# Kernel optimization log

Hardware: AMD Instinct MI355X
Metric: run time of the kernel (lower is better)

## Reference

```python
import jax, jax.numpy as jnp
import numpy as np

B, H, S, DK = 2, 16, 2048, 64


def setup_inputs() -> dict:
    key = jax.random.key(0)
    kq, kk, kv = jax.random.split(key, 3)
    Q = jax.random.normal(kq, (B, H, S, DK), dtype=jnp.float32)
    K = jax.random.normal(kk, (B, H, S, DK), dtype=jnp.float32)
    V = jax.random.normal(kv, (B, H, S, DK), dtype=jnp.float32)
    mask = jnp.tril(jnp.ones((S, S), dtype=bool))  # causal, broadcasts over (B, H)
    return {"Q": Q, "K": K, "V": V, "mask": mask}


def reference(Q, K, V, mask):
    d_k = Q.shape[-1]
    scale = 1.0 / jnp.sqrt(jnp.asarray(d_k, dtype=Q.dtype))
    # [..., m, n] attention scores
    qk = jnp.einsum("bhmd,bhnd->bhmn", Q, K) * scale
    qk = jnp.where(mask, qk, -jnp.inf)
    attn = jax.nn.softmax(qk, axis=-1)
    return jnp.einsum("bhmn,bhnd->bhmd", attn, V)
```

## Files before the change

kernel.cpp:

```cpp
#include <hip/hip_runtime.h>
#include <hip/hip_bf16.h>
#include <stdint.h>


#define SEQ   2048
#define DKK   64
#define KVB   64
#define NKT   (SEQ / KVB)
#define TILE_BYTES 16384
#define WS_NEED ((size_t)32 * NKT * TILE_BYTES)

typedef float  f32x4  __attribute__((ext_vector_type(4)));
typedef short  s16x8  __attribute__((ext_vector_type(8)));
typedef short  s16x4  __attribute__((ext_vector_type(4)));
typedef __bf16 bf16x8 __attribute__((ext_vector_type(8)));

static __device__ __forceinline__ unsigned short f2b(float x) {
  union { float f; uint32_t u; } v; v.f = x;
  uint32_t r = v.u + 0x7fffu + ((v.u >> 16) & 1u);
  return (unsigned short)(r >> 16);
}

static __device__ __forceinline__ int swzA(int row, int col) {
  return row * 128 + ((((col >> 3) ^ (row & 7)) << 4)) + ((col & 7) << 1);
}
static __device__ __forceinline__ int swzV(int d, int kv) {
  return d * 128 + ((((kv >> 3) ^ ((d >> 1) & 7)) << 4)) + ((kv & 7) << 1);
}

__global__ __launch_bounds__(256)
void prep_kv(const float* __restrict__ Kg, const float* __restrict__ Vg,
             char* __restrict__ ws) {
  const int b   = blockIdx.x;
  const int bh  = b >> 5, kt = b & 31;
  const int tid = threadIdx.x;
  char* tile = ws + ((size_t)b << 14);
  const size_t base = ((size_t)bh * SEQ + (size_t)kt * KVB) * DKK;
  const float* Kb = Kg + base;
  const float* Vb = Vg + base;
  {
    int col4 = tid & 15, rq = tid >> 4;
#pragma unroll
    for (int ii = 0; ii < 4; ++ii) {
      int row = ii * 16 + rq;
      f32x4 v = *(const f32x4*)(Kb + (size_t)row * DKK + col4 * 4);
      s16x4 w; w[0]=f2b(v[0]); w[1]=f2b(v[1]); w[2]=f2b(v[2]); w[3]=f2b(v[3]);
      *(s16x4*)(tile + swzA(row, col4 * 4)) = w;
    }
  }
  {
    int d0 = (tid & 15) * 4, kv0 = (tid >> 4) * 4;
    f32x4 vv[4];
#pragma unroll
    for (int r2 = 0; r2 < 4; ++r2)
      vv[r2] = *(const f32x4*)(Vb + (size_t)(kv0 + r2) * DKK + d0);
#pragma unroll
    for (int j = 0; j < 4; ++j) {
      s16x4 w; w[0]=f2b(vv[0][j]); w[1]=f2b(vv[1][j]); w[2]=f2b(vv[2][j]); w[3]=f2b(vv[3][j]);
      *(s16x4*)(tile + 8192 + swzV(d0 + j, kv0)) = w;
    }
  }
}

__global__ __launch_bounds__(256, 2)
void attn_fwd5(const float* __restrict__ Qg, const char* __restrict__ ws,
               float* __restrict__ Og) {
  __shared__ __align__(16) char smem[TILE_BYTES + 4 * 2048];

  const int tid  = threadIdx.x;
  const int lane = tid & 63;
  const int wave = tid >> 6;
  const int c    = lane & 15;
  const int g    = lane >> 4;

  const int f     = blockIdx.x;
  const int xcd   = f & 7;
  const int inner = f >> 3;
  const int bh    = ((inner >> 4) << 3) | xcd;
  const int p     = inner & 15;
  const int qt_a  = 31 - p;
  const int qt_b  = p;
  const int nkt_a = qt_a + 1;
  const int nkt_b = qt_b + 1;

  const float CS = 0.18033688011f;
  const size_t bhoff = (size_t)bh * SEQ * DKK;
  const float* Qb = Qg + bhoff;
  float*       Ob = Og + bhoff;
  const char*  wsb = ws + ((size_t)bh * NKT << 14);

  s16x8 stA0 = *(const s16x8*)(wsb + tid * 16);
  s16x8 stA1 = *(const s16x8*)(wsb + 4096 + tid * 16);
  s16x8 stB0 = *(const s16x8*)(wsb + 8192 + tid * 16);
  s16x8 stB1 = *(const s16x8*)(wsb + 12288 + tid * 16);

  s16x8 qfA[2], qfB[2];
#pragma unroll
  for (int h = 0; h < 2; ++h) {
    int d0 = h * 32 + g * 8;
    {
      const f32x4* pq = (const f32x4*)(Qb + (size_t)(qt_a * 64 + wave * 16 + c) * DKK + d0);
      f32x4 a = pq[0], b = pq[1];
      s16x8 r;
      r[0]=f2b(a[0]*CS); r[1]=f2b(a[1]*CS); r[2]=f2b(a[2]*CS); r[3]=f2b(a[3]*CS);
      r[4]=f2b(b[0]*CS); r[5]=f2b(b[1]*CS); r[6]=f2b(b[2]*CS); r[7]=f2b(b[3]*CS);
      qfA[h] = r;
    }
    {
      const f32x4* pq = (const f32x4*)(Qb + (size_t)(qt_b * 64 + wave * 16 + c) * DKK + d0);
      f32x4 a = pq[0], b = pq[1];
      s16x8 r;
      r[0]=f2b(a[0]*CS); r[1]=f2b(a[1]*CS); r[2]=f2b(a[2]*CS); r[3]=f2b(a[3]*CS);
      r[4]=f2b(b[0]*CS); r[5]=f2b(b[1]*CS); r[6]=f2b(b[2]*CS); r[7]=f2b(b[3]*CS);
      qfB[h] = r;
    }
  }

  s16x8 ones8;
#pragma unroll
  for (int j = 0; j < 8; ++j) ones8[j] = (short)0x3F80;

  f32x4 OA[4] = {}, OB[4] = {};
  f32x4 OlA = {}, OlB = {};

  char* Kl = smem;
  char* Vl = smem + 8192;
  char* Pl = smem + TILE_BYTES + wave * 2048;

  auto compute_tile = [&](const s16x8* qf, f32x4* O, f32x4& Ol, bool domask) {
    f32x4 S[4] = {};
    __builtin_amdgcn_s_setprio(1);
#pragma unroll
    for (int s = 0; s < 4; ++s)
#pragma unroll
      for (int h = 0; h < 2; ++h) {
        s16x8 kf = *(const s16x8*)(Kl + swzA(s * 16 + c, h * 32 + g * 8));
        S[s] = __builtin_amdgcn_mfma_f32_16x16x32_bf16(
            __builtin_bit_cast(bf16x8, qf[h]),
            __builtin_bit_cast(bf16x8, kf), S[s], 0, 0, 0);
      }
    __builtin_amdgcn_s_setprio(0);

    if (domask) {
      int qrl = wave * 16 + g * 4;
#pragma unroll
      for (int s = 0; s < 4; ++s) {
        int kvl = s * 16 + c;
#pragma unroll
        for (int r = 0; r < 4; ++r)
          if (kvl > qrl + r) S[s][r] = -1e30f;
      }
    }

#pragma unroll
    for (int r = 0; r < 4; ++r)
#pragma unroll
      for (int s = 0; s < 4; ++s) {
        float pv = exp2f(S[s][r]);
        *(unsigned short*)(Pl + swzA(g * 4 + r, s * 16 + c)) = f2b(pv);
      }

    __builtin_amdgcn_s_setprio(1);
#pragma unroll
    for (int ch = 0; ch < 2; ++ch) {
      s16x8 pa = *(const s16x8*)(Pl + swzA(c, ch * 32 + g * 8));
#pragma unroll
      for (int t = 0; t < 4; ++t) {
        s16x8 vb = *(const s16x8*)(Vl + swzV(t * 16 + c, ch * 32 + g * 8));
        O[t] = __builtin_amdgcn_mfma_f32_16x16x32_bf16(
            __builtin_bit_cast(bf16x8, pa),
            __builtin_bit_cast(bf16x8, vb), O[t], 0, 0, 0);
      }
      Ol = __builtin_amdgcn_mfma_f32_16x16x32_bf16(
          __builtin_bit_cast(bf16x8, pa),
          __builtin_bit_cast(bf16x8, ones8), Ol, 0, 0, 0);
    }
    __builtin_amdgcn_s_setprio(0);
  };

  for (int kt = 0; kt < nkt_a; ++kt) {
    __syncthreads();
    *(s16x8*)(smem + tid * 16)         = stA0;
    *(s16x8*)(smem + 4096 + tid * 16)  = stA1;
    *(s16x8*)(smem + 8192 + tid * 16)  = stB0;
    *(s16x8*)(smem + 12288 + tid * 16) = stB1;
    if (kt + 1 < nkt_a) {
      const char* tn = wsb + ((size_t)(kt + 1) << 14);
      stA0 = *(const s16x8*)(tn + tid * 16);
      stA1 = *(const s16x8*)(tn + 4096 + tid * 16);
      stB0 = *(const s16x8*)(tn + 8192 + tid * 16);
      stB1 = *(const s16x8*)(tn + 12288 + tid * 16);
    }
    __syncthreads();

    compute_tile(qfA, OA, OlA, kt == qt_a);
    if (kt < nkt_b)
      compute_tile(qfB, OB, OlB, kt == qt_b);
  }

#pragma unroll
  for (int r = 0; r < 4; ++r) {
    int qra = qt_a * 64 + wave * 16 + g * 4 + r;
    int qrb = qt_b * 64 + wave * 16 + g * 4 + r;
    float ia = 1.f / OlA[r];
    float ib = 1.f / OlB[r];
#pragma unroll
    for (int t = 0; t < 4; ++t) {
      Ob[(size_t)qra * DKK + t * 16 + c] = OA[t][r] * ia;
      Ob[(size_t)qrb * DKK + t * 16 + c] = OB[t][r] * ib;
    }
  }
}

__global__ __launch_bounds__(256, 2)
void attn_fwd(const float* __restrict__ Qg, const float* __restrict__ Kg,
              const float* __restrict__ Vg, float* __restrict__ Og) {
  __shared__ __align__(16) char smem[8192 + 8192 + 8 * 2048];
  char* Kl = smem;
  char* Vl = smem + 8192;
  const int tid  = threadIdx.x;
  const int lane = tid & 63;
  const int wave = tid >> 6;
  const int c    = lane & 15;
  const int g    = lane >> 4;
  const int f    = blockIdx.x;
  const int xcd  = f & 7;
  const int inner= f >> 3;
  const int bh   = ((inner >> 4) << 3) | xcd;
  const int qt   = 15 - (inner & 15);
  const float CS = 0.18033688011f;
  const size_t bhoff = (size_t)bh * SEQ * DKK;
  const float* Qb = Qg + bhoff;
  const float* Kb = Kg + bhoff;
  const float* Vb = Vg + bhoff;
  float*       Ob = Og + bhoff;
  s16x8 qf[2][2];
#pragma unroll
  for (int u = 0; u < 2; ++u) {
    int qrow = qt * 128 + wave * 32 + u * 16 + c;
#pragma unroll
    for (int h = 0; h < 2; ++h) {
      int d0 = h * 32 + g * 8;
      const f32x4* pq = (const f32x4*)(Qb + (size_t)qrow * DKK + d0);
      f32x4 a = pq[0], b = pq[1];
      s16x8 r;
      r[0]=f2b(a[0]*CS); r[1]=f2b(a[1]*CS); r[2]=f2b(a[2]*CS); r[3]=f2b(a[3]*CS);
      r[4]=f2b(b[0]*CS); r[5]=f2b(b[1]*CS); r[6]=f2b(b[2]*CS); r[7]=f2b(b[3]*CS);
      qf[u][h] = r;
    }
  }
  f32x4 O[2][4] = {};
  float m[2][4], l[2][4];
#pragma unroll
  for (int u = 0; u < 2; ++u)
#pragma unroll
    for (int r = 0; r < 4; ++r) { m[u][r] = -1e30f; l[u][r] = 0.f; }
  const int nkt = 2 * qt + 2;
  for (int kt = 0; kt < nkt; ++kt) {
    __syncthreads();
    {
      int col4 = tid & 15, rq = tid >> 4;
#pragma unroll
      for (int ii = 0; ii < 4; ++ii) {
        int row = ii * 16 + rq;
        f32x4 v = *(const f32x4*)(Kb + (size_t)(kt * KVB + row) * DKK + col4 * 4);
        s16x4 w; w[0]=f2b(v[0]); w[1]=f2b(v[1]); w[2]=f2b(v[2]); w[3]=f2b(v[3]);
        *(s16x4*)(Kl + swzA(row, col4 * 4)) = w;
      }
      int d0 = (tid & 15) * 4, kv0 = (tid >> 4) * 4;
      f32x4 vv[4];
#pragma unroll
      for (int r2 = 0; r2 < 4; ++r2)
        vv[r2] = *(const f32x4*)(Vb + (size_t)(kt * KVB + kv0 + r2) * DKK + d0);
#pragma unroll
      for (int j = 0; j < 4; ++j) {
        s16x4 w; w[0]=f2b(vv[0][j]); w[1]=f2b(vv[1][j]); w[2]=f2b(vv[2][j]); w[3]=f2b(vv[3][j]);
        *(s16x4*)(Vl + swzV(d0 + j, kv0)) = w;
      }
    }
    __syncthreads();
    f32x4 S[2][4] = {};
#pragma unroll
    for (int s = 0; s < 4; ++s)
#pragma unroll
      for (int h = 0; h < 2; ++h) {
        s16x8 kf = *(const s16x8*)(Kl + swzA(s * 16 + c, h * 32 + g * 8));
#pragma unroll
        for (int u = 0; u < 2; ++u)
          S[u][s] = __builtin_amdgcn_mfma_f32_16x16x32_bf16(
              __builtin_bit_cast(bf16x8, qf[u][h]),
              __builtin_bit_cast(bf16x8, kf), S[u][s], 0, 0, 0);
      }
    if (kt >= nkt - 2) {
#pragma unroll
      for (int u = 0; u < 2; ++u) {
        int qrb = qt * 128 + wave * 32 + u * 16 + g * 4;
#pragma unroll
        for (int s = 0; s < 4; ++s) {
          int kv = kt * KVB + s * 16 + c;
#pragma unroll
          for (int r = 0; r < 4; ++r)
            if (kv > qrb + r) S[u][s][r] = -1e30f;
        }
      }
    }
#pragma unroll
    for (int u = 0; u < 2; ++u) {
      char* Pl = smem + 16384 + (wave * 2 + u) * 2048;
#pragma unroll
      for (int r = 0; r < 4; ++r) {
        float t0 = fmaxf(fmaxf(S[u][0][r], S[u][1][r]),
                         fmaxf(S[u][2][r], S[u][3][r]));
#pragma unroll
        for (int off = 1; off <= 8; off <<= 1)
          t0 = fmaxf(t0, __shfl_xor(t0, off));
        float mn   = fmaxf(m[u][r], t0);
        float corr = exp2f(m[u][r] - mn);
        float ps = 0.f;
#pragma unroll
        for (int s = 0; s < 4; ++s) {
          float pv = exp2f(S[u][s][r] - mn);
          ps += pv;
          *(unsigned short*)(Pl + swzA(g * 4 + r, s * 16 + c)) = f2b(pv);
        }
#pragma unroll
        for (int off = 1; off <= 8; off <<= 1)
          ps += __shfl_xor(ps, off);
        l[u][r] = l[u][r] * corr + ps;
        m[u][r] = mn;
#pragma unroll
        for (int t = 0; t < 4; ++t) O[u][t][r] *= corr;
      }
    }
#pragma unroll
    for (int ch = 0; ch < 2; ++ch) {
      s16x8 pa[2];
#pragma unroll
      for (int u = 0; u < 2; ++u)
        pa[u] = *(const s16x8*)(smem + 16384 + (wave * 2 + u) * 2048
                                + swzA(c, ch * 32 + g * 8));
#pragma unroll
      for (int t = 0; t < 4; ++t) {
        s16x8 vb = *(const s16x8*)(Vl + swzV(t * 16 + c, ch * 32 + g * 8));
#pragma unroll
        for (int u = 0; u < 2; ++u)
          O[u][t] = __builtin_amdgcn_mfma_f32_16x16x32_bf16(
              __builtin_bit_cast(bf16x8, pa[u]),
              __builtin_bit_cast(bf16x8, vb), O[u][t], 0, 0, 0);
      }
    }
  }
#pragma unroll
  for (int u = 0; u < 2; ++u)
#pragma unroll
    for (int r = 0; r < 4; ++r) {
      int qrow = qt * 128 + wave * 32 + u * 16 + g * 4 + r;
      float inv = 1.f / l[u][r];
#pragma unroll
      for (int t = 0; t < 4; ++t)
        Ob[(size_t)qrow * DKK + t * 16 + c] = O[u][t][r] * inv;
    }
}

extern "C" void kernel_launch(void* const* d_in, const int* in_sizes, int n_in,
                              void* d_out, int out_size, void* d_ws, size_t ws_size,
                              hipStream_t stream) {
  const float* Q = (const float*)d_in[0];
  const float* K = (const float*)d_in[1];
  const float* V = (const float*)d_in[2];
  float* O = (float*)d_out;
  (void)in_sizes; (void)n_in; (void)out_size;
  if (ws_size >= WS_NEED) {
    char* ws = (char*)d_ws;
    prep_kv<<<dim3(32 * NKT), dim3(256), 0, stream>>>(K, V, ws);
    attn_fwd5<<<dim3(512), dim3(256), 0, stream>>>(Q, ws, O);
  } else {
    attn_fwd<<<dim3(512), dim3(256), 0, stream>>>(Q, K, V, O);
  }
}
```

Baseline: 58.39 us.

## Split KV range across two blocks per query pair with atomic reduction

Splits each query-pair's KV loop between two blocks (even and odd tiles), doubling the grid to 1024 blocks and raising the launch-bounds occupancy hint to 4. Partial outputs and row sums are accumulated with float atomics into a zeroed output and a row-sum workspace, and a separate normalization kernel then divides by the row sums. This targets load imbalance and low occupancy, at the cost of two memsets, an extra kernel launch, atomic traffic, and a larger workspace requirement. The old fused non-workspace fallback kernel is removed, and the fallback path now runs prep_kv even when the workspace may be too small.

```diff
diff --git a/kernel.cpp b/kernel.cpp
--- a/kernel.cpp
+++ b/kernel.cpp
@@ -8,7 +8,10 @@
 #define KVB   64
 #define NKT   (SEQ / KVB)
 #define TILE_BYTES 16384
-#define WS_NEED ((size_t)32 * NKT * TILE_BYTES)
+#define WS_TILES ((size_t)32 * NKT * TILE_BYTES)
+#define L_BYTES  ((size_t)32 * SEQ * 4)
+#define WS_NEED  WS_TILES
+#define WS_NEED2 (WS_TILES + L_BYTES)
 
 typedef float  f32x4  __attribute__((ext_vector_type(4)));
 typedef short  s16x8  __attribute__((ext_vector_type(8)));
@@ -62,9 +65,9 @@
   }
 }
 
-__global__ __launch_bounds__(256, 2)
-void attn_fwd5(const float* __restrict__ Qg, const char* __restrict__ ws,
-               float* __restrict__ Og) {
+__global__ __launch_bounds__(256, 4)
+void attn_fwd6(const float* __restrict__ Qg, const char* __restrict__ ws,
+               float* __restrict__ lws, float* __restrict__ Og) {
   __shared__ __align__(16) char smem[TILE_BYTES + 4 * 2048];
 
   const int tid  = threadIdx.x;
@@ -73,6 +76,175 @@
   const int c    = lane & 15;
   const int g    = lane >> 4;
 
+  const int f      = blockIdx.x;
+  const int xcd    = f & 7;
+  const int inner  = f >> 3;
+  const int half   = inner & 1;
+  const int inner2 = inner >> 1;
+  const int bh     = ((inner2 >> 4) << 3) | xcd;
+  const int p      = inner2 & 15;
+  const int qt_a   = 31 - p;
+  const int qt_b   = p;
+  const int nkt_a  = qt_a + 1;
+  const int nkt_b  = qt_b + 1;
+
+  const float CS = 0.18033688011f;
+  const size_t bhoff = (size_t)bh * SEQ * DKK;
+  const float* Qb = Qg + bhoff;
+  float*       Ob = Og + bhoff;
+  float*       lbh = lws + bh * SEQ;
+  const char*  wsb = ws + ((size_t)bh * NKT << 14);
+
+  {
+  }
+  const char* t0p = wsb + ((size_t)half << 14);
+  s16x8 stA0 = *(const s16x8*)(t0p + tid * 16);
+  s16x8 stA1 = *(const s16x8*)(t0p + 4096 + tid * 16);
+  s16x8 stB0 = *(const s16x8*)(t0p + 8192 + tid * 16);
+  s16x8 stB1 = *(const s16x8*)(t0p + 12288 + tid * 16);
+
+  s16x8 qfA[2], qfB[2];
+#pragma unroll
+  for (int h = 0; h < 2; ++h) {
+    int d0 = h * 32 + g * 8;
+    {
+      const f32x4* pq = (const f32x4*)(Qb + (size_t)(qt_a * 64 + wave * 16 + c) * DKK + d0);
+      f32x4 a = pq[0], b = pq[1];
+      s16x8 r;
+      r[0]=f2b(a[0]*CS); r[1]=f2b(a[1]*CS); r[2]=f2b(a[2]*CS); r[3]=f2b(a[3]*CS);
+      r[4]=f2b(b[0]*CS); r[5]=f2b(b[1]*CS); r[6]=f2b(b[2]*CS); r[7]=f2b(b[3]*CS);
+      qfA[h] = r;
+    }
+    {
+      const f32x4* pq = (const f32x4*)(Qb + (size_t)(qt_b * 64 + wave * 16 + c) * DKK + d0);
+      f32x4 a = pq[0], b = pq[1];
+      s16x8 r;
+      r[0]=f2b(a[0]*CS); r[1]=f2b(a[1]*CS); r[2]=f2b(a[2]*CS); r[3]=f2b(a[3]*CS);
+      r[4]=f2b(b[0]*CS); r[5]=f2b(b[1]*CS); r[6]=f2b(b[2]*CS); r[7]=f2b(b[3]*CS);
+      qfB[h] = r;
+    }
+  }
+
+  s16x8 ones8;
+#pragma unroll
+  for (int j = 0; j < 8; ++j) ones8[j] = (short)0x3F80;
+
+  f32x4 OA[4] = {}, OB[4] = {};
+  f32x4 OlA = {}, OlB = {};
+
+  char* Kl = smem;
+  char* Vl = smem + 8192;
+  char* Pl = smem + TILE_BYTES + wave * 2048;
+
+  auto compute_tile = [&](const s16x8* qf, f32x4* O, f32x4& Ol, bool domask) {
+    f32x4 S[4] = {};
+    __builtin_amdgcn_s_setprio(1);
+#pragma unroll
+    for (int s = 0; s < 4; ++s)
+#pragma unroll
+      for (int h = 0; h < 2; ++h) {
+        s16x8 kf = *(const s16x8*)(Kl + swzA(s * 16 + c, h * 32 + g * 8));
+        S[s] = __builtin_amdgcn_mfma_f32_16x16x32_bf16(
+            __builtin_bit_cast(bf16x8, qf[h]),
+            __builtin_bit_cast(bf16x8, kf), S[s], 0, 0, 0);
+      }
+    __builtin_amdgcn_s_setprio(0);
+
+    if (domask) {
+      int qrl = wave * 16 + g * 4;
+#pragma unroll
+      for (int s = 0; s < 4; ++s) {
+        int kvl = s * 16 + c;
+#pragma unroll
+        for (int r = 0; r < 4; ++r)
+          if (kvl > qrl + r) S[s][r] = -1e30f;
+      }
+    }
+
+#pragma unroll
+    for (int r = 0; r < 4; ++r)
+#pragma unroll
+      for (int s = 0; s < 4; ++s) {
+        float pv = exp2f(S[s][r]);
+        *(unsigned short*)(Pl + swzA(g * 4 + r, s * 16 + c)) = f2b(pv);
+      }
+
+    __builtin_amdgcn_s_setprio(1);
+#pragma unroll
+    for (int ch = 0; ch < 2; ++ch) {
+      s16x8 pa = *(const s16x8*)(Pl + swzA(c, ch * 32 + g * 8));
+#pragma unroll
+      for (int t = 0; t < 4; ++t) {
+        s16x8 vb = *(const s16x8*)(Vl + swzV(t * 16 + c, ch * 32 + g * 8));
+        O[t] = __builtin_amdgcn_mfma_f32_16x16x32_bf16(
+            __builtin_bit_cast(bf16x8, pa),
+            __builtin_bit_cast(bf16x8, vb), O[t], 0, 0, 0);
+      }
+      Ol = __builtin_amdgcn_mfma_f32_16x16x32_bf16(
+          __builtin_bit_cast(bf16x8, pa),
+          __builtin_bit_cast(bf16x8, ones8), Ol, 0, 0, 0);
+    }
+    __builtin_amdgcn_s_setprio(0);
+  };
+
+  for (int kt = half; kt < nkt_a; kt += 2) {
+    __syncthreads();
+    *(s16x8*)(smem + tid * 16)         = stA0;
+    *(s16x8*)(smem + 4096 + tid * 16)  = stA1;
+    *(s16x8*)(smem + 8192 + tid * 16)  = stB0;
+    *(s16x8*)(smem + 12288 + tid * 16) = stB1;
+    if (kt + 2 < nkt_a) {
+      const char* tn = wsb + ((size_t)(kt + 2) << 14);
+      stA0 = *(const s16x8*)(tn + tid * 16);
+      stA1 = *(const s16x8*)(tn + 4096 + tid * 16);
+      stB0 = *(const s16x8*)(tn + 8192 + tid * 16);
+      stB1 = *(const s16x8*)(tn + 12288 + tid * 16);
+    }
+    __syncthreads();
+
+    compute_tile(qfA, OA, OlA, kt == qt_a);
+    if (kt < nkt_b)
+      compute_tile(qfB, OB, OlB, kt == qt_b);
+  }
+
+#pragma unroll
+  for (int r = 0; r < 4; ++r) {
+    int qra = qt_a * 64 + wave * 16 + g * 4 + r;
+    int qrb = qt_b * 64 + wave * 16 + g * 4 + r;
+#pragma unroll
+    for (int t = 0; t < 4; ++t) {
+      atomicAdd(&Ob[(size_t)qra * DKK + t * 16 + c], OA[t][r]);
+      atomicAdd(&Ob[(size_t)qrb * DKK + t * 16 + c], OB[t][r]);
+    }
+    if (c == 0) {
+      atomicAdd(&lbh[qra], OlA[r]);
+      atomicAdd(&lbh[qrb], OlB[r]);
+    }
+  }
+}
+
+__global__ __launch_bounds__(256)
+void norm_out(float* __restrict__ Og, const float* __restrict__ lws) {
+  const int gid = blockIdx.x * 256 + threadIdx.x;
+  const size_t base = (size_t)gid * 8;
+  const int row = (int)(base >> 6);
+  float inv = 1.f / lws[row];
+  f32x4* p = (f32x4*)(Og + base);
+  f32x4 a = p[0], b = p[1];
+#pragma unroll
+  for (int j = 0; j < 4; ++j) { a[j] *= inv; b[j] *= inv; }
+  p[0] = a; p[1] = b;
+}
+
+__global__ __launch_bounds__(256, 2)
+void attn_fwd5(const float* __restrict__ Qg, const char* __restrict__ ws,
+               float* __restrict__ Og) {
+  __shared__ __align__(16) char smem[TILE_BYTES + 4 * 2048];
+  const int tid  = threadIdx.x;
+  const int lane = tid & 63;
+  const int wave = tid >> 6;
+  const int c    = lane & 15;
+  const int g    = lane >> 4;
   const int f     = blockIdx.x;
   const int xcd   = f & 7;
   const int inner = f >> 3;
@@ -82,18 +254,15 @@
   const int qt_b  = p;
   const int nkt_a = qt_a + 1;
   const int nkt_b = qt_b + 1;
-
   const float CS = 0.18033688011f;
   const size_t bhoff = (size_t)bh * SEQ * DKK;
   const float* Qb = Qg + bhoff;
   float*       Ob = Og + bhoff;
   const char*  wsb = ws + ((size_t)bh * NKT << 14);
-
   s16x8 stA0 = *(const s16x8*)(wsb + tid * 16);
   s16x8 stA1 = *(const s16x8*)(wsb + 4096 + tid * 16);
   s16x8 stB0 = *(const s16x8*)(wsb + 8192 + tid * 16);
   s16x8 stB1 = *(const s16x8*)(wsb + 12288 + tid * 16);
-
   s16x8 qfA[2], qfB[2];
 #pragma unroll
   for (int h = 0; h < 2; ++h) {
@@ -115,21 +284,16 @@
       qfB[h] = r;
     }
   }
-
   s16x8 ones8;
 #pragma unroll
   for (int j = 0; j < 8; ++j) ones8[j] = (short)0x3F80;
-
   f32x4 OA[4] = {}, OB[4] = {};
   f32x4 OlA = {}, OlB = {};
-
   char* Kl = smem;
   char* Vl = smem + 8192;
   char* Pl = smem + TILE_BYTES + wave * 2048;
-
   auto compute_tile = [&](const s16x8* qf, f32x4* O, f32x4& Ol, bool domask) {
     f32x4 S[4] = {};
-    __builtin_amdgcn_s_setprio(1);
 #pragma unroll
     for (int s = 0; s < 4; ++s)
 #pragma unroll
@@ -139,8 +303,6 @@
             __builtin_bit_cast(bf16x8, qf[h]),
             __builtin_bit_cast(bf16x8, kf), S[s], 0, 0, 0);
       }
-    __builtin_amdgcn_s_setprio(0);
-
     if (domask) {
       int qrl = wave * 16 + g * 4;
 #pragma unroll
@@ -151,7 +313,6 @@
           if (kvl > qrl + r) S[s][r] = -1e30f;
       }
     }
-
 #pragma unroll
     for (int r = 0; r < 4; ++r)
 #pragma unroll
@@ -159,8 +320,6 @@
         float pv = exp2f(S[s][r]);
         *(unsigned short*)(Pl + swzA(g * 4 + r, s * 16 + c)) = f2b(pv);
       }
-
-    __builtin_amdgcn_s_setprio(1);
 #pragma unroll
     for (int ch = 0; ch < 2; ++ch) {
       s16x8 pa = *(const s16x8*)(Pl + swzA(c, ch * 32 + g * 8));
@@ -175,9 +334,7 @@
           __builtin_bit_cast(bf16x8, pa),
           __builtin_bit_cast(bf16x8, ones8), Ol, 0, 0, 0);
     }
-    __builtin_amdgcn_s_setprio(0);
   };
-
   for (int kt = 0; kt < nkt_a; ++kt) {
     __syncthreads();
     *(s16x8*)(smem + tid * 16)         = stA0;
@@ -192,12 +349,10 @@
       stB1 = *(const s16x8*)(tn + 12288 + tid * 16);
     }
     __syncthreads();
-
     compute_tile(qfA, OA, OlA, kt == qt_a);
     if (kt < nkt_b)
       compute_tile(qfB, OB, OlB, kt == qt_b);
   }
-
 #pragma unroll
   for (int r = 0; r < 4; ++r) {
     int qra = qt_a * 64 + wave * 16 + g * 4 + r;
@@ -210,156 +365,6 @@
       Ob[(size_t)qrb * DKK + t * 16 + c] = OB[t][r] * ib;
     }
   }
-}
-
-__global__ __launch_bounds__(256, 2)
-void attn_fwd(const float* __restrict__ Qg, const float* __restrict__ Kg,
-              const float* __restrict__ Vg, float* __restrict__ Og) {
-  __shared__ __align__(16) char smem[8192 + 8192 + 8 * 2048];
-  char* Kl = smem;
-  char* Vl = smem + 8192;
-  const int tid  = threadIdx.x;
-  const int lane = tid & 63;
-  const int wave = tid >> 6;
-  const int c    = lane & 15;
-  const int g    = lane >> 4;
-  const int f    = blockIdx.x;
-  const int xcd  = f & 7;
-  const int inner= f >> 3;
-  const int bh   = ((inner >> 4) << 3) | xcd;
-  const int qt   = 15 - (inner & 15);
-  const float CS = 0.18033688011f;
-  const size_t bhoff = (size_t)bh * SEQ * DKK;
-  const float* Qb = Qg + bhoff;
-  const float* Kb = Kg + bhoff;
-  const float* Vb = Vg + bhoff;
-  float*       Ob = Og + bhoff;
-  s16x8 qf[2][2];
-#pragma unroll
-  for (int u = 0; u < 2; ++u) {
-    int qrow = qt * 128 + wave * 32 + u * 16 + c;
-#pragma unroll
-    for (int h = 0; h < 2; ++h) {
-      int d0 = h * 32 + g * 8;
-      const f32x4* pq = (const f32x4*)(Qb + (size_t)qrow * DKK + d0);
-      f32x4 a = pq[0], b = pq[1];
-      s16x8 r;
-      r[0]=f2b(a[0]*CS); r[1]=f2b(a[1]*CS); r[2]=f2b(a[2]*CS); r[3]=f2b(a[3]*CS);
-      r[4]=f2b(b[0]*CS); r[5]=f2b(b[1]*CS); r[6]=f2b(b[2]*CS); r[7]=f2b(b[3]*CS);
-      qf[u][h] = r;
-    }
-  }
-  f32x4 O[2][4] = {};
-  float m[2][4], l[2][4];
-#pragma unroll
-  for (int u = 0; u < 2; ++u)
-#pragma unroll
-    for (int r = 0; r < 4; ++r) { m[u][r] = -1e30f; l[u][r] = 0.f; }
-  const int nkt = 2 * qt + 2;
-  for (int kt = 0; kt < nkt; ++kt) {
-    __syncthreads();
-    {
-      int col4 = tid & 15, rq = tid >> 4;
-#pragma unroll
-      for (int ii = 0; ii < 4; ++ii) {
-        int row = ii * 16 + rq;
-        f32x4 v = *(const f32x4*)(Kb + (size_t)(kt * KVB + row) * DKK + col4 * 4);
-        s16x4 w; w[0]=f2b(v[0]); w[1]=f2b(v[1]); w[2]=f2b(v[2]); w[3]=f2b(v[3]);
-        *(s16x4*)(Kl + swzA(row, col4 * 4)) = w;
-      }
-      int d0 = (tid & 15) * 4, kv0 = (tid >> 4) * 4;
-      f32x4 vv[4];
-#pragma unroll
-      for (int r2 = 0; r2 < 4; ++r2)
-        vv[r2] = *(const f32x4*)(Vb + (size_t)(kt * KVB + kv0 + r2) * DKK + d0);
-#pragma unroll
-      for (int j = 0; j < 4; ++j) {
-        s16x4 w; w[0]=f2b(vv[0][j]); w[1]=f2b(vv[1][j]); w[2]=f2b(vv[2][j]); w[3]=f2b(vv[3][j]);
-        *(s16x4*)(Vl + swzV(d0 + j, kv0)) = w;
-      }
-    }
-    __syncthreads();
-    f32x4 S[2][4] = {};
-#pragma unroll
-    for (int s = 0; s < 4; ++s)
-#pragma unroll
-      for (int h = 0; h < 2; ++h) {
-        s16x8 kf = *(const s16x8*)(Kl + swzA(s * 16 + c, h * 32 + g * 8));
-#pragma unroll
-        for (int u = 0; u < 2; ++u)
-          S[u][s] = __builtin_amdgcn_mfma_f32_16x16x32_bf16(
-              __builtin_bit_cast(bf16x8, qf[u][h]),
-              __builtin_bit_cast(bf16x8, kf), S[u][s], 0, 0, 0);
-      }
-    if (kt >= nkt - 2) {
-#pragma unroll
-      for (int u = 0; u < 2; ++u) {
-        int qrb = qt * 128 + wave * 32 + u * 16 + g * 4;
-#pragma unroll
-        for (int s = 0; s < 4; ++s) {
-          int kv = kt * KVB + s * 16 + c;
-#pragma unroll
-          for (int r = 0; r < 4; ++r)
-            if (kv > qrb + r) S[u][s][r] = -1e30f;
-        }
-      }
-    }
-#pragma unroll
-    for (int u = 0; u < 2; ++u) {
-      char* Pl = smem + 16384 + (wave * 2 + u) * 2048;
-#pragma unroll
-      for (int r = 0; r < 4; ++r) {
-        float t0 = fmaxf(fmaxf(S[u][0][r], S[u][1][r]),
-                         fmaxf(S[u][2][r], S[u][3][r]));
-#pragma unroll
-        for (int off = 1; off <= 8; off <<= 1)
-          t0 = fmaxf(t0, __shfl_xor(t0, off));
-        float mn   = fmaxf(m[u][r], t0);
-        float corr = exp2f(m[u][r] - mn);
-        float ps = 0.f;
-#pragma unroll
-        for (int s = 0; s < 4; ++s) {
-          float pv = exp2f(S[u][s][r] - mn);
-          ps += pv;
-          *(unsigned short*)(Pl + swzA(g * 4 + r, s * 16 + c)) = f2b(pv);
-        }
-#pragma unroll
-        for (int off = 1; off <= 8; off <<= 1)
-          ps += __shfl_xor(ps, off);
-        l[u][r] = l[u][r] * corr + ps;
-        m[u][r] = mn;
-#pragma unroll
-        for (int t = 0; t < 4; ++t) O[u][t][r] *= corr;
-      }
-    }
-#pragma unroll
-    for (int ch = 0; ch < 2; ++ch) {
-      s16x8 pa[2];
-#pragma unroll
-      for (int u = 0; u < 2; ++u)
-        pa[u] = *(const s16x8*)(smem + 16384 + (wave * 2 + u) * 2048
-                                + swzA(c, ch * 32 + g * 8));
-#pragma unroll
-      for (int t = 0; t < 4; ++t) {
-        s16x8 vb = *(const s16x8*)(Vl + swzV(t * 16 + c, ch * 32 + g * 8));
-#pragma unroll
-        for (int u = 0; u < 2; ++u)
-          O[u][t] = __builtin_amdgcn_mfma_f32_16x16x32_bf16(
-              __builtin_bit_cast(bf16x8, pa[u]),
-              __builtin_bit_cast(bf16x8, vb), O[u][t], 0, 0, 0);
-      }
-    }
-  }
-#pragma unroll
-  for (int u = 0; u < 2; ++u)
-#pragma unroll
-    for (int r = 0; r < 4; ++r) {
-      int qrow = qt * 128 + wave * 32 + u * 16 + g * 4 + r;
-      float inv = 1.f / l[u][r];
-#pragma unroll
-      for (int t = 0; t < 4; ++t)
-        Ob[(size_t)qrow * DKK + t * 16 + c] = O[u][t][r] * inv;
-    }
 }
 
 extern "C" void kernel_launch(void* const* d_in, const int* in_sizes, int n_in,
@@ -369,12 +374,17 @@
   const float* K = (const float*)d_in[1];
   const float* V = (const float*)d_in[2];
   float* O = (float*)d_out;
-  (void)in_sizes; (void)n_in; (void)out_size;
-  if (ws_size >= WS_NEED) {
-    char* ws = (char*)d_ws;
+  (void)in_sizes; (void)n_in;
+  char* ws = (char*)d_ws;
+  if (ws_size >= WS_NEED2) {
+    float* lws = (float*)(ws + WS_TILES);
+    hipMemsetAsync(d_out, 0, (size_t)out_size * sizeof(float), stream);
+    hipMemsetAsync(lws, 0, L_BYTES, stream);
+    prep_kv<<<dim3(32 * NKT), dim3(256), 0, stream>>>(K, V, ws);
+    attn_fwd6<<<dim3(1024), dim3(256), 0, stream>>>(Q, ws, lws, O);
+    norm_out<<<dim3((unsigned)(((size_t)out_size / 8 + 255) / 256)), dim3(256), 0, stream>>>(O, lws);
+  } else {
     prep_kv<<<dim3(32 * NKT), dim3(256), 0, stream>>>(K, V, ws);
     attn_fwd5<<<dim3(512), dim3(256), 0, stream>>>(Q, ws, O);
-  } else {
-    attn_fwd<<<dim3(512), dim3(256), 0, stream>>>(Q, K, V, O);
-  }
-}
+  }
+}
```

Measured after the change: 80.99 us. +38.7%, slower.

## Split attention waves 2x2 over query rows and KV halves with cross-wave reduction

Applied to the files above, without the earlier changes.

Changes the wave decomposition in the main attention kernel. Instead of each wave owning 16 query rows over all 64 KV columns, waves form a 2x2 grid: each owns 32 query rows and half of the KV tile. K fragments are then loaded once per wave and reused across two query sub-tiles. The V tile in the prep kernel is reordered to match the new P layout, and partial O and row-sum results from the two KV halves are combined through shared memory at the end. This is meant to improve K/V fragment reuse and MFMA density per LDS read, at the cost of a larger P buffer, more registers, and extra barriers plus a shared-memory reduction in the epilogue.

```diff
diff --git a/kernel.cpp b/kernel.cpp
--- a/kernel.cpp
+++ b/kernel.cpp
@@ -24,8 +24,8 @@
 static __device__ __forceinline__ int swzA(int row, int col) {
   return row * 128 + ((((col >> 3) ^ (row & 7)) << 4)) + ((col & 7) << 1);
 }
-static __device__ __forceinline__ int swzV(int d, int kv) {
-  return d * 128 + ((((kv >> 3) ^ ((d >> 1) & 7)) << 4)) + ((kv & 7) << 1);
+static __device__ __forceinline__ int swzV(int d, int pos) {
+  return d * 128 + ((((pos >> 3) ^ ((d >> 1) & 7)) << 4)) + ((pos & 7) << 1);
 }
 
 __global__ __launch_bounds__(256)
@@ -49,29 +49,34 @@
     }
   }
   {
-    int d0 = (tid & 15) * 4, kv0 = (tid >> 4) * 4;
+    int d0 = (tid & 15) * 4, pos0 = (tid >> 4) * 4;
+    int half = pos0 >> 5, p0 = pos0 & 31;
+    int kvb = half * 32 + (p0 >> 1);
     f32x4 vv[4];
-#pragma unroll
-    for (int r2 = 0; r2 < 4; ++r2)
-      vv[r2] = *(const f32x4*)(Vb + (size_t)(kv0 + r2) * DKK + d0);
+    vv[0] = *(const f32x4*)(Vb + (size_t)(kvb)      * DKK + d0);
+    vv[1] = *(const f32x4*)(Vb + (size_t)(kvb + 16) * DKK + d0);
+    vv[2] = *(const f32x4*)(Vb + (size_t)(kvb + 1)  * DKK + d0);
+    vv[3] = *(const f32x4*)(Vb + (size_t)(kvb + 17) * DKK + d0);
 #pragma unroll
     for (int j = 0; j < 4; ++j) {
       s16x4 w; w[0]=f2b(vv[0][j]); w[1]=f2b(vv[1][j]); w[2]=f2b(vv[2][j]); w[3]=f2b(vv[3][j]);
-      *(s16x4*)(tile + 8192 + swzV(d0 + j, kv0)) = w;
+      *(s16x4*)(tile + 8192 + swzV(d0 + j, pos0)) = w;
     }
   }
 }
 
 __global__ __launch_bounds__(256, 2)
-void attn_fwd5(const float* __restrict__ Qg, const char* __restrict__ ws,
+void attn_fwd8(const float* __restrict__ Qg, const char* __restrict__ ws,
                float* __restrict__ Og) {
-  __shared__ __align__(16) char smem[TILE_BYTES + 4 * 2048];
+  __shared__ __align__(16) char smem[TILE_BYTES + 4 * 4096];
 
   const int tid  = threadIdx.x;
   const int lane = tid & 63;
   const int wave = tid >> 6;
   const int c    = lane & 15;
   const int g    = lane >> 4;
+  const int wq   = wave >> 1;
+  const int wk   = wave & 1;
 
   const int f     = blockIdx.x;
   const int xcd   = f & 7;
@@ -89,132 +94,212 @@
   float*       Ob = Og + bhoff;
   const char*  wsb = ws + ((size_t)bh * NKT << 14);
 
-  s16x8 stA0 = *(const s16x8*)(wsb + tid * 16);
-  s16x8 stA1 = *(const s16x8*)(wsb + 4096 + tid * 16);
-  s16x8 stB0 = *(const s16x8*)(wsb + 8192 + tid * 16);
-  s16x8 stB1 = *(const s16x8*)(wsb + 12288 + tid * 16);
-
-  s16x8 qfA[2], qfB[2];
-#pragma unroll
-  for (int h = 0; h < 2; ++h) {
-    int d0 = h * 32 + g * 8;
-    {
-      const f32x4* pq = (const f32x4*)(Qb + (size_t)(qt_a * 64 + wave * 16 + c) * DKK + d0);
-      f32x4 a = pq[0], b = pq[1];
-      s16x8 r;
-      r[0]=f2b(a[0]*CS); r[1]=f2b(a[1]*CS); r[2]=f2b(a[2]*CS); r[3]=f2b(a[3]*CS);
-      r[4]=f2b(b[0]*CS); r[5]=f2b(b[1]*CS); r[6]=f2b(b[2]*CS); r[7]=f2b(b[3]*CS);
-      qfA[h] = r;
-    }
-    {
-      const f32x4* pq = (const f32x4*)(Qb + (size_t)(qt_b * 64 + wave * 16 + c) * DKK + d0);
-      f32x4 a = pq[0], b = pq[1];
-      s16x8 r;
-      r[0]=f2b(a[0]*CS); r[1]=f2b(a[1]*CS); r[2]=f2b(a[2]*CS); r[3]=f2b(a[3]*CS);
-      r[4]=f2b(b[0]*CS); r[5]=f2b(b[1]*CS); r[6]=f2b(b[2]*CS); r[7]=f2b(b[3]*CS);
-      qfB[h] = r;
-    }
-  }
+  s16x8 st0 = *(const s16x8*)(wsb + tid * 16);
+  s16x8 st1 = *(const s16x8*)(wsb + 4096 + tid * 16);
+  s16x8 st2 = *(const s16x8*)(wsb + 8192 + tid * 16);
+  s16x8 st3 = *(const s16x8*)(wsb + 12288 + tid * 16);
+
+  s16x8 qfA[2][2], qfB[2][2];
+#pragma unroll
+  for (int uu = 0; uu < 2; ++uu)
+#pragma unroll
+    for (int h = 0; h < 2; ++h) {
+      int d0 = h * 32 + g * 8;
+      {
+        const f32x4* pq = (const f32x4*)(Qb + (size_t)(qt_a * 64 + (wq * 2 + uu) * 16 + c) * DKK + d0);
+        f32x4 a = pq[0], b = pq[1];
+        s16x8 r;
+        r[0]=f2b(a[0]*CS); r[1]=f2b(a[1]*CS); r[2]=f2b(a[2]*CS); r[3]=f2b(a[3]*CS);
+        r[4]=f2b(b[0]*CS); r[5]=f2b(b[1]*CS); r[6]=f2b(b[2]*CS); r[7]=f2b(b[3]*CS);
+        qfA[uu][h] = r;
+      }
+      {
+        const f32x4* pq = (const f32x4*)(Qb + (size_t)(qt_b * 64 + (wq * 2 + uu) * 16 + c) * DKK + d0);
+        f32x4 a = pq[0], b = pq[1];
+        s16x8 r;
+        r[0]=f2b(a[0]*CS); r[1]=f2b(a[1]*CS); r[2]=f2b(a[2]*CS); r[3]=f2b(a[3]*CS);
+        r[4]=f2b(b[0]*CS); r[5]=f2b(b[1]*CS); r[6]=f2b(b[2]*CS); r[7]=f2b(b[3]*CS);
+        qfB[uu][h] = r;
+      }
+    }
 
   s16x8 ones8;
 #pragma unroll
   for (int j = 0; j < 8; ++j) ones8[j] = (short)0x3F80;
 
-  f32x4 OA[4] = {}, OB[4] = {};
-  f32x4 OlA = {}, OlB = {};
+  f32x4 OA[2][4] = {}, OB[2][4] = {};
+  f32x4 OlA[2] = {}, OlB[2] = {};
 
   char* Kl = smem;
   char* Vl = smem + 8192;
-  char* Pl = smem + TILE_BYTES + wave * 2048;
-
-  auto compute_tile = [&](const s16x8* qf, f32x4* O, f32x4& Ol, bool domask) {
-    f32x4 S[4] = {};
-    __builtin_amdgcn_s_setprio(1);
-#pragma unroll
-    for (int s = 0; s < 4; ++s)
-#pragma unroll
-      for (int h = 0; h < 2; ++h) {
-        s16x8 kf = *(const s16x8*)(Kl + swzA(s * 16 + c, h * 32 + g * 8));
-        S[s] = __builtin_amdgcn_mfma_f32_16x16x32_bf16(
-            __builtin_bit_cast(bf16x8, qf[h]),
-            __builtin_bit_cast(bf16x8, kf), S[s], 0, 0, 0);
-      }
-    __builtin_amdgcn_s_setprio(0);
-
-    if (domask) {
-      int qrl = wave * 16 + g * 4;
-#pragma unroll
-      for (int s = 0; s < 4; ++s) {
-        int kvl = s * 16 + c;
-#pragma unroll
-        for (int r = 0; r < 4; ++r)
-          if (kvl > qrl + r) S[s][r] = -1e30f;
-      }
-    }
-
-#pragma unroll
-    for (int r = 0; r < 4; ++r)
-#pragma unroll
-      for (int s = 0; s < 4; ++s) {
-        float pv = exp2f(S[s][r]);
-        *(unsigned short*)(Pl + swzA(g * 4 + r, s * 16 + c)) = f2b(pv);
-      }
-
-    __builtin_amdgcn_s_setprio(1);
-#pragma unroll
-    for (int ch = 0; ch < 2; ++ch) {
-      s16x8 pa = *(const s16x8*)(Pl + swzA(c, ch * 32 + g * 8));
-#pragma unroll
-      for (int t = 0; t < 4; ++t) {
-        s16x8 vb = *(const s16x8*)(Vl + swzV(t * 16 + c, ch * 32 + g * 8));
-        O[t] = __builtin_amdgcn_mfma_f32_16x16x32_bf16(
-            __builtin_bit_cast(bf16x8, pa),
-            __builtin_bit_cast(bf16x8, vb), O[t], 0, 0, 0);
-      }
-      Ol = __builtin_amdgcn_mfma_f32_16x16x32_bf16(
-          __builtin_bit_cast(bf16x8, pa),
-          __builtin_bit_cast(bf16x8, ones8), Ol, 0, 0, 0);
-    }
-    __builtin_amdgcn_s_setprio(0);
-  };
+  char* Pl = smem + TILE_BYTES + wave * 4096;
+  const int pwSwz = (c * 4) ^ ((g & 1) << 5);
+  const int prOff = c * 64 + ((g * 16) ^ ((c & 3) << 4) ^ (((c >> 2) & 1) << 5));
 
   for (int kt = 0; kt < nkt_a; ++kt) {
     __syncthreads();
-    *(s16x8*)(smem + tid * 16)         = stA0;
-    *(s16x8*)(smem + 4096 + tid * 16)  = stA1;
-    *(s16x8*)(smem + 8192 + tid * 16)  = stB0;
-    *(s16x8*)(smem + 12288 + tid * 16) = stB1;
+    *(s16x8*)(smem + tid * 16)         = st0;
+    *(s16x8*)(smem + 4096 + tid * 16)  = st1;
+    *(s16x8*)(smem + 8192 + tid * 16)  = st2;
+    *(s16x8*)(smem + 12288 + tid * 16) = st3;
     if (kt + 1 < nkt_a) {
       const char* tn = wsb + ((size_t)(kt + 1) << 14);
-      stA0 = *(const s16x8*)(tn + tid * 16);
-      stA1 = *(const s16x8*)(tn + 4096 + tid * 16);
-      stB0 = *(const s16x8*)(tn + 8192 + tid * 16);
-      stB1 = *(const s16x8*)(tn + 12288 + tid * 16);
-    }
-    __syncthreads();
-
-    compute_tile(qfA, OA, OlA, kt == qt_a);
-    if (kt < nkt_b)
-      compute_tile(qfB, OB, OlB, kt == qt_b);
-  }
-
-#pragma unroll
-  for (int r = 0; r < 4; ++r) {
-    int qra = qt_a * 64 + wave * 16 + g * 4 + r;
-    int qrb = qt_b * 64 + wave * 16 + g * 4 + r;
-    float ia = 1.f / OlA[r];
-    float ib = 1.f / OlB[r];
+      st0 = *(const s16x8*)(tn + tid * 16);
+      st1 = *(const s16x8*)(tn + 4096 + tid * 16);
+      st2 = *(const s16x8*)(tn + 8192 + tid * 16);
+      st3 = *(const s16x8*)(tn + 12288 + tid * 16);
+    }
+    __syncthreads();
+
+    const bool doB = (kt < nkt_b);
+
+    s16x8 kf[2][2];
+#pragma unroll
+    for (int sl = 0; sl < 2; ++sl)
+#pragma unroll
+      for (int h = 0; h < 2; ++h)
+        kf[sl][h] = *(const s16x8*)(Kl + swzA((wk * 2 + sl) * 16 + c, h * 32 + g * 8));
+
+    f32x4 SA[2][2] = {}, SB[2][2] = {};
+    __builtin_amdgcn_s_setprio(1);
+#pragma unroll
+    for (int uu = 0; uu < 2; ++uu)
+#pragma unroll
+      for (int sl = 0; sl < 2; ++sl)
+#pragma unroll
+        for (int h = 0; h < 2; ++h)
+          SA[uu][sl] = __builtin_amdgcn_mfma_f32_16x16x32_bf16(
+              __builtin_bit_cast(bf16x8, qfA[uu][h]),
+              __builtin_bit_cast(bf16x8, kf[sl][h]), SA[uu][sl], 0, 0, 0);
+    if (doB) {
+#pragma unroll
+      for (int uu = 0; uu < 2; ++uu)
+#pragma unroll
+        for (int sl = 0; sl < 2; ++sl)
+#pragma unroll
+          for (int h = 0; h < 2; ++h)
+            SB[uu][sl] = __builtin_amdgcn_mfma_f32_16x16x32_bf16(
+                __builtin_bit_cast(bf16x8, qfB[uu][h]),
+                __builtin_bit_cast(bf16x8, kf[sl][h]), SB[uu][sl], 0, 0, 0);
+    }
+    __builtin_amdgcn_s_setprio(0);
+
+    if (kt == qt_a) {
+#pragma unroll
+      for (int uu = 0; uu < 2; ++uu)
+#pragma unroll
+        for (int sl = 0; sl < 2; ++sl) {
+          int kvl = wk * 32 + sl * 16 + c;
+#pragma unroll
+          for (int r = 0; r < 4; ++r)
+            if (kvl > (wq * 2 + uu) * 16 + g * 4 + r) SA[uu][sl][r] = -1e30f;
+        }
+    }
+    if (doB && kt == qt_b) {
+#pragma unroll
+      for (int uu = 0; uu < 2; ++uu)
+#pragma unroll
+        for (int sl = 0; sl < 2; ++sl) {
+          int kvl = wk * 32 + sl * 16 + c;
+#pragma unroll
+          for (int r = 0; r < 4; ++r)
+            if (kvl > (wq * 2 + uu) * 16 + g * 4 + r) SB[uu][sl][r] = -1e30f;
+        }
+    }
+
+#pragma unroll
+    for (int uu = 0; uu < 2; ++uu)
+#pragma unroll
+      for (int r = 0; r < 4; ++r) {
+        uint32_t w = (uint32_t)f2b(exp2f(SA[uu][0][r]))
+                   | ((uint32_t)f2b(exp2f(SA[uu][1][r])) << 16);
+        *(uint32_t*)(Pl + uu * 1024 + (g * 4 + r) * 64 + (pwSwz ^ (r << 4))) = w;
+      }
+    if (doB) {
+#pragma unroll
+      for (int uu = 0; uu < 2; ++uu)
+#pragma unroll
+        for (int r = 0; r < 4; ++r) {
+          uint32_t w = (uint32_t)f2b(exp2f(SB[uu][0][r]))
+                     | ((uint32_t)f2b(exp2f(SB[uu][1][r])) << 16);
+          *(uint32_t*)(Pl + (2 + uu) * 1024 + (g * 4 + r) * 64 + (pwSwz ^ (r << 4))) = w;
+        }
+    }
+
+    s16x8 paA0 = *(const s16x8*)(Pl + 0 * 1024 + prOff);
+    s16x8 paA1 = *(const s16x8*)(Pl + 1 * 1024 + prOff);
+    s16x8 paB0, paB1;
+    if (doB) {
+      paB0 = *(const s16x8*)(Pl + 2 * 1024 + prOff);
+      paB1 = *(const s16x8*)(Pl + 3 * 1024 + prOff);
+    }
+    __builtin_amdgcn_s_setprio(1);
 #pragma unroll
     for (int t = 0; t < 4; ++t) {
-      Ob[(size_t)qra * DKK + t * 16 + c] = OA[t][r] * ia;
-      Ob[(size_t)qrb * DKK + t * 16 + c] = OB[t][r] * ib;
-    }
-  }
+      s16x8 vb = *(const s16x8*)(Vl + swzV(t * 16 + c, wk * 32 + g * 8));
+      OA[0][t] = __builtin_amdgcn_mfma_f32_16x16x32_bf16(
+          __builtin_bit_cast(bf16x8, paA0), __builtin_bit_cast(bf16x8, vb), OA[0][t], 0, 0, 0);
+      OA[1][t] = __builtin_amdgcn_mfma_f32_16x16x32_bf16(
+          __builtin_bit_cast(bf16x8, paA1), __builtin_bit_cast(bf16x8, vb), OA[1][t], 0, 0, 0);
+      if (doB) {
+        OB[0][t] = __builtin_amdgcn_mfma_f32_16x16x32_bf16(
+            __builtin_bit_cast(bf16x8, paB0), __builtin_bit_cast(bf16x8, vb), OB[0][t], 0, 0, 0);
+        OB[1][t] = __builtin_amdgcn_mfma_f32_16x16x32_bf16(
+            __builtin_bit_cast(bf16x8, paB1), __builtin_bit_cast(bf16x8, vb), OB[1][t], 0, 0, 0);
+      }
+    }
+    OlA[0] = __builtin_amdgcn_mfma_f32_16x16x32_bf16(
+        __builtin_bit_cast(bf16x8, paA0), __builtin_bit_cast(bf16x8, ones8), OlA[0], 0, 0, 0);
+    OlA[1] = __builtin_amdgcn_mfma_f32_16x16x32_bf16(
+        __builtin_bit_cast(bf16x8, paA1), __builtin_bit_cast(bf16x8, ones8), OlA[1], 0, 0, 0);
+    if (doB) {
+      OlB[0] = __builtin_amdgcn_mfma_f32_16x16x32_bf16(
+          __builtin_bit_cast(bf16x8, paB0), __builtin_bit_cast(bf16x8, ones8), OlB[0], 0, 0, 0);
+      OlB[1] = __builtin_amdgcn_mfma_f32_16x16x32_bf16(
+          __builtin_bit_cast(bf16x8, paB1), __builtin_bit_cast(bf16x8, ones8), OlB[1], 0, 0, 0);
+    }
+    __builtin_amdgcn_s_setprio(0);
+  }
+
+  __syncthreads();
+  auto reduce_store = [&](f32x4 (&O)[2][4], f32x4 (&Ol)[2], int qt) {
+    if (wk == 1) {
+#pragma unroll
+      for (int uu = 0; uu < 2; ++uu) {
+#pragma unroll
+        for (int t = 0; t < 4; ++t)
+          *(f32x4*)(smem + ((((wq * 2 + uu) * 5 + t) * 64 + lane) << 4)) = O[uu][t];
+        *(f32x4*)(smem + ((((wq * 2 + uu) * 5 + 4) * 64 + lane) << 4)) = Ol[uu];
+      }
+    }
+    __syncthreads();
+    if (wk == 0) {
+#pragma unroll
+      for (int uu = 0; uu < 2; ++uu) {
+        f32x4 l2 = Ol[uu] + *(const f32x4*)(smem + ((((wq * 2 + uu) * 5 + 4) * 64 + lane) << 4));
+        f32x4 inv;
+#pragma unroll
+        for (int r = 0; r < 4; ++r) inv[r] = 1.f / l2[r];
+#pragma unroll
+        for (int t = 0; t < 4; ++t) {
+          f32x4 o = O[uu][t] + *(const f32x4*)(smem + ((((wq * 2 + uu) * 5 + t) * 64 + lane) << 4));
+#pragma unroll
+          for (int r = 0; r < 4; ++r) {
+            int qrow = qt * 64 + (wq * 2 + uu) * 16 + g * 4 + r;
+            Ob[(size_t)qrow * DKK + t * 16 + c] = o[r] * inv[r];
+          }
+        }
+      }
+    }
+    __syncthreads();
+  };
+  reduce_store(OA, OlA, qt_a);
+  reduce_store(OB, OlB, qt_b);
 }
 
 __global__ __launch_bounds__(256, 2)
-void attn_fwd(const float* __restrict__ Qg, const float* __restrict__ Kg,
-              const float* __restrict__ Vg, float* __restrict__ Og) {
+void attn_fwd_fb(const float* __restrict__ Qg, const float* __restrict__ Kg,
+                 const float* __restrict__ Vg, float* __restrict__ Og) {
   __shared__ __align__(16) char smem[8192 + 8192 + 8 * 2048];
   char* Kl = smem;
   char* Vl = smem + 8192;
@@ -373,8 +458,8 @@
   if (ws_size >= WS_NEED) {
     char* ws = (char*)d_ws;
     prep_kv<<<dim3(32 * NKT), dim3(256), 0, stream>>>(K, V, ws);
-    attn_fwd5<<<dim3(512), dim3(256), 0, stream>>>(Q, ws, O);
+    attn_fwd8<<<dim3(512), dim3(256), 0, stream>>>(Q, ws, O);
   } else {
-    attn_fwd<<<dim3(512), dim3(256), 0, stream>>>(Q, K, V, O);
-  }
-}
+    attn_fwd_fb<<<dim3(512), dim3(256), 0, stream>>>(Q, K, V, O);
+  }
+}
```

Result: slower. 65.43 us (+12.0%).

## Interleave two query tiles per KV tile, use direct global-to-LDS loads and packed bf16 P

Applied to the files above, without the earlier changes.

Replaces the register-staged prefetch of K/V tiles with global_load_lds direct-to-LDS copies, followed by a full vmcnt wait each iteration. The two query tiles' QK and PV MFMAs are interleaved in one loop body with separate P buffers to expose more independent MFMA work. P is written with packed v_cvt_pk_bf16_f32 stores in a new swizzle, and the V tile layout is permuted in prep to match. The cost is losing the overlap of the next tile's load with the current tile's compute, and using more LDS per block.

```diff
diff --git a/kernel.cpp b/kernel.cpp
--- a/kernel.cpp
+++ b/kernel.cpp
@@ -24,8 +24,20 @@
 static __device__ __forceinline__ int swzA(int row, int col) {
   return row * 128 + ((((col >> 3) ^ (row & 7)) << 4)) + ((col & 7) << 1);
 }
-static __device__ __forceinline__ int swzV(int d, int kv) {
-  return d * 128 + ((((kv >> 3) ^ ((d >> 1) & 7)) << 4)) + ((kv & 7) << 1);
+static __device__ __forceinline__ int swzV(int d, int pos) {
+  return d * 128 + ((((pos >> 3) ^ ((d >> 1) & 7)) << 4)) + ((pos & 7) << 1);
+}
+
+static __device__ __forceinline__ void gload16(const void* g, void* l) {
+  __builtin_amdgcn_global_load_lds(
+      (const __attribute__((address_space(1))) void*)g,
+      (__attribute__((address_space(3))) void*)l, 16, 0, 0);
+}
+
+static __device__ __forceinline__ uint32_t cvtpk(float s0, float s1) {
+  uint32_t r;
+  asm("v_cvt_pk_bf16_f32 %0, %1, %2" : "=v"(r) : "v"(s0), "v"(s1));
+  return r;
 }
 
 __global__ __launch_bounds__(256)
@@ -49,23 +61,26 @@
     }
   }
   {
-    int d0 = (tid & 15) * 4, kv0 = (tid >> 4) * 4;
+    int d0 = (tid & 15) * 4, pos0 = (tid >> 4) * 4;
+    int half = pos0 >> 5, p0 = pos0 & 31;
+    int kvb = half * 32 + (p0 >> 1);
     f32x4 vv[4];
-#pragma unroll
-    for (int r2 = 0; r2 < 4; ++r2)
-      vv[r2] = *(const f32x4*)(Vb + (size_t)(kv0 + r2) * DKK + d0);
+    vv[0] = *(const f32x4*)(Vb + (size_t)(kvb)      * DKK + d0);
+    vv[1] = *(const f32x4*)(Vb + (size_t)(kvb + 16) * DKK + d0);
+    vv[2] = *(const f32x4*)(Vb + (size_t)(kvb + 1)  * DKK + d0);
+    vv[3] = *(const f32x4*)(Vb + (size_t)(kvb + 17) * DKK + d0);
 #pragma unroll
     for (int j = 0; j < 4; ++j) {
       s16x4 w; w[0]=f2b(vv[0][j]); w[1]=f2b(vv[1][j]); w[2]=f2b(vv[2][j]); w[3]=f2b(vv[3][j]);
-      *(s16x4*)(tile + 8192 + swzV(d0 + j, kv0)) = w;
+      *(s16x4*)(tile + 8192 + swzV(d0 + j, pos0)) = w;
     }
   }
 }
 
 __global__ __launch_bounds__(256, 2)
-void attn_fwd5(const float* __restrict__ Qg, const char* __restrict__ ws,
+void attn_fwd9(const float* __restrict__ Qg, const char* __restrict__ ws,
                float* __restrict__ Og) {
-  __shared__ __align__(16) char smem[TILE_BYTES + 4 * 2048];
+  __shared__ __align__(16) char smem[TILE_BYTES + 4 * 4096];
 
   const int tid  = threadIdx.x;
   const int lane = tid & 63;
@@ -89,11 +104,6 @@
   float*       Ob = Og + bhoff;
   const char*  wsb = ws + ((size_t)bh * NKT << 14);
 
-  s16x8 stA0 = *(const s16x8*)(wsb + tid * 16);
-  s16x8 stA1 = *(const s16x8*)(wsb + 4096 + tid * 16);
-  s16x8 stB0 = *(const s16x8*)(wsb + 8192 + tid * 16);
-  s16x8 stB1 = *(const s16x8*)(wsb + 12288 + tid * 16);
-
   s16x8 qfA[2], qfB[2];
 #pragma unroll
   for (int h = 0; h < 2; ++h) {
@@ -125,77 +135,100 @@
 
   char* Kl = smem;
   char* Vl = smem + 8192;
-  char* Pl = smem + TILE_BYTES + wave * 2048;
-
-  auto compute_tile = [&](const s16x8* qf, f32x4* O, f32x4& Ol, bool domask) {
-    f32x4 S[4] = {};
+  char* PA = smem + TILE_BYTES + wave * 4096;
+  char* PB = PA + 2048;
+  const int prOff0 = c * 128 + ((g * 16) ^ ((c & 3) << 4) ^ (((c >> 2) & 1) << 5));
+
+  for (int kt = 0; kt < nkt_a; ++kt) {
+    __syncthreads();
+    {
+      const char* tn = wsb + ((size_t)kt << 14);
+#pragma unroll
+      for (int j = 0; j < 4; ++j)
+        gload16(tn + wave * 4096 + j * 1024 + lane * 16,
+                smem + wave * 4096 + j * 1024);
+    }
+    asm volatile("s_waitcnt vmcnt(0)" ::: "memory");
+    __syncthreads();
+
+    const bool doB = (kt < nkt_b);
+
+    f32x4 SA[4] = {}, SB[4] = {};
     __builtin_amdgcn_s_setprio(1);
 #pragma unroll
     for (int s = 0; s < 4; ++s)
 #pragma unroll
       for (int h = 0; h < 2; ++h) {
         s16x8 kf = *(const s16x8*)(Kl + swzA(s * 16 + c, h * 32 + g * 8));
-        S[s] = __builtin_amdgcn_mfma_f32_16x16x32_bf16(
-            __builtin_bit_cast(bf16x8, qf[h]),
-            __builtin_bit_cast(bf16x8, kf), S[s], 0, 0, 0);
+        SA[s] = __builtin_amdgcn_mfma_f32_16x16x32_bf16(
+            __builtin_bit_cast(bf16x8, qfA[h]),
+            __builtin_bit_cast(bf16x8, kf), SA[s], 0, 0, 0);
+        if (doB)
+          SB[s] = __builtin_amdgcn_mfma_f32_16x16x32_bf16(
+              __builtin_bit_cast(bf16x8, qfB[h]),
+              __builtin_bit_cast(bf16x8, kf), SB[s], 0, 0, 0);
       }
     __builtin_amdgcn_s_setprio(0);
 
-    if (domask) {
+    if (kt == qt_a) {
       int qrl = wave * 16 + g * 4;
 #pragma unroll
       for (int s = 0; s < 4; ++s) {
         int kvl = s * 16 + c;
 #pragma unroll
         for (int r = 0; r < 4; ++r)
-          if (kvl > qrl + r) S[s][r] = -1e30f;
-      }
-    }
-
-#pragma unroll
-    for (int r = 0; r < 4; ++r)
+          if (kvl > qrl + r) SA[s][r] = -1e30f;
+      }
+    }
+    if (doB && kt == qt_b) {
+      int qrl = wave * 16 + g * 4;
 #pragma unroll
       for (int s = 0; s < 4; ++s) {
-        float pv = exp2f(S[s][r]);
-        *(unsigned short*)(Pl + swzA(g * 4 + r, s * 16 + c)) = f2b(pv);
-      }
+        int kvl = s * 16 + c;
+#pragma unroll
+        for (int r = 0; r < 4; ++r)
+          if (kvl > qrl + r) SB[s][r] = -1e30f;
+      }
+    }
+
+#pragma unroll
+    for (int r = 0; r < 4; ++r) {
+      int wr = (g * 4 + r) * 128 + ((c * 4) ^ (r << 4) ^ ((g & 1) << 5));
+      *(uint32_t*)(PA + wr)        = cvtpk(exp2f(SA[0][r]), exp2f(SA[1][r]));
+      *(uint32_t*)(PA + (wr ^ 64)) = cvtpk(exp2f(SA[2][r]), exp2f(SA[3][r]));
+    }
+    if (doB) {
+#pragma unroll
+      for (int r = 0; r < 4; ++r) {
+        int wr = (g * 4 + r) * 128 + ((c * 4) ^ (r << 4) ^ ((g & 1) << 5));
+        *(uint32_t*)(PB + wr)        = cvtpk(exp2f(SB[0][r]), exp2f(SB[1][r]));
+        *(uint32_t*)(PB + (wr ^ 64)) = cvtpk(exp2f(SB[2][r]), exp2f(SB[3][r]));
+      }
+    }
 
     __builtin_amdgcn_s_setprio(1);
 #pragma unroll
     for (int ch = 0; ch < 2; ++ch) {
-      s16x8 pa = *(const s16x8*)(Pl + swzA(c, ch * 32 + g * 8));
+      int pr = prOff0 ^ (ch << 6);
+      s16x8 paA = *(const s16x8*)(PA + pr);
+      s16x8 paB;
+      if (doB) paB = *(const s16x8*)(PB + pr);
 #pragma unroll
       for (int t = 0; t < 4; ++t) {
         s16x8 vb = *(const s16x8*)(Vl + swzV(t * 16 + c, ch * 32 + g * 8));
-        O[t] = __builtin_amdgcn_mfma_f32_16x16x32_bf16(
-            __builtin_bit_cast(bf16x8, pa),
-            __builtin_bit_cast(bf16x8, vb), O[t], 0, 0, 0);
-      }
-      Ol = __builtin_amdgcn_mfma_f32_16x16x32_bf16(
-          __builtin_bit_cast(bf16x8, pa),
-          __builtin_bit_cast(bf16x8, ones8), Ol, 0, 0, 0);
+        OA[t] = __builtin_amdgcn_mfma_f32_16x16x32_bf16(
+            __builtin_bit_cast(bf16x8, paA), __builtin_bit_cast(bf16x8, vb), OA[t], 0, 0, 0);
+        if (doB)
+          OB[t] = __builtin_amdgcn_mfma_f32_16x16x32_bf16(
+              __builtin_bit_cast(bf16x8, paB), __builtin_bit_cast(bf16x8, vb), OB[t], 0, 0, 0);
+      }
+      OlA = __builtin_amdgcn_mfma_f32_16x16x32_bf16(
+          __builtin_bit_cast(bf16x8, paA), __builtin_bit_cast(bf16x8, ones8), OlA, 0, 0, 0);
+      if (doB)
+        OlB = __builtin_amdgcn_mfma_f32_16x16x32_bf16(
+            __builtin_bit_cast(bf16x8, paB), __builtin_bit_cast(bf16x8, ones8), OlB, 0, 0, 0);
     }
     __builtin_amdgcn_s_setprio(0);
-  };
-
-  for (int kt = 0; kt < nkt_a; ++kt) {
-    __syncthreads();
-    *(s16x8*)(smem + tid * 16)         = stA0;
-    *(s16x8*)(smem + 4096 + tid * 16)  = stA1;
-    *(s16x8*)(smem + 8192 + tid * 16)  = stB0;
-    *(s16x8*)(smem + 12288 + tid * 16) = stB1;
-    if (kt + 1 < nkt_a) {
-      const char* tn = wsb + ((size_t)(kt + 1) << 14);
-      stA0 = *(const s16x8*)(tn + tid * 16);
-      stA1 = *(const s16x8*)(tn + 4096 + tid * 16);
-      stB0 = *(const s16x8*)(tn + 8192 + tid * 16);
-      stB1 = *(const s16x8*)(tn + 12288 + tid * 16);
-    }
-    __syncthreads();
-
-    compute_tile(qfA, OA, OlA, kt == qt_a);
-    if (kt < nkt_b)
-      compute_tile(qfB, OB, OlB, kt == qt_b);
   }
 
 #pragma unroll
@@ -213,8 +246,8 @@
 }
 
 __global__ __launch_bounds__(256, 2)
-void attn_fwd(const float* __restrict__ Qg, const float* __restrict__ Kg,
-              const float* __restrict__ Vg, float* __restrict__ Og) {
+void attn_fwd_fb(const float* __restrict__ Qg, const float* __restrict__ Kg,
+                 const float* __restrict__ Vg, float* __restrict__ Og) {
   __shared__ __align__(16) char smem[8192 + 8192 + 8 * 2048];
   char* Kl = smem;
   char* Vl = smem + 8192;
@@ -373,8 +406,8 @@
   if (ws_size >= WS_NEED) {
     char* ws = (char*)d_ws;
     prep_kv<<<dim3(32 * NKT), dim3(256), 0, stream>>>(K, V, ws);
-    attn_fwd5<<<dim3(512), dim3(256), 0, stream>>>(Q, ws, O);
+    attn_fwd9<<<dim3(512), dim3(256), 0, stream>>>(Q, ws, O);
   } else {
-    attn_fwd<<<dim3(512), dim3(256), 0, stream>>>(Q, K, V, O);
-  }
-}
+    attn_fwd_fb<<<dim3(512), dim3(256), 0, stream>>>(Q, K, V, O);
+  }
+}
```

Result: slower. 69.42 us (+18.9%).
